# Kernel optimization log

Measured on AMD Instinct MI355X. Metric: run time of the kernel, lower is better.

Reference implementation:

```python
import jax, jax.numpy as jnp
import numpy as np

B, N, C, L = 2, 128, 256, 3
NODE_IN, EDGE_IN = 128, 64
KN, KE = 101, 7
ALPHA = 0.2
EPS = 1e-5

def lrelu(x):
    return jax.nn.leaky_relu(x, ALPHA)

def layer_norm(x, g, b):
    mu = jnp.mean(x, axis=-1, keepdims=True)
    var = jnp.mean((x - mu) ** 2, axis=-1, keepdims=True)
    return (x - mu) / jnp.sqrt(var + EPS) * g + b

def setup_inputs() -> dict:
    key = jax.random.key(0)
    ks = jax.random.split(key, 20)
    s = 0.05
    nodes = jax.random.normal(ks[0], (B, N, NODE_IN), jnp.float32)
    edges = jax.random.normal(ks[1], (B, N, N, EDGE_IN), jnp.float32)
    m = (jax.random.uniform(ks[2], (B, N, N)) > 0.3).astype(jnp.float32)
    adj_mask = jnp.maximum(m, jnp.eye(N, dtype=jnp.float32)[None])  # guarantee non-empty rows
    return {
        'nodes': nodes, 'edges': edges, 'adj_mask': adj_mask,
        'pnW': jax.random.normal(ks[3], (C, NODE_IN)) * s, 'pnb': jnp.zeros((C,)),
        'peW': jax.random.normal(ks[4], (C, EDGE_IN)) * s, 'peb': jnp.zeros((C,)),
        'Wb': jax.random.normal(ks[5], (L, C, 3 * C)) * s,
        'Wbp': jax.random.normal(ks[6], (L, C, C)) * s,
        'Wfp': jax.random.normal(ks[7], (L, C, C)) * s,
        'ub': jax.random.normal(ks[8], (L, C)) * s,
        'Wf': jax.random.normal(ks[9], (L, C, C)) * s,
        'eln_g': jnp.ones((L, C)), 'eln_b': jnp.zeros((L, C)),
        'nln_g': jnp.ones((L, C)), 'nln_b': jnp.zeros((L, C)),
        'ncW': jax.random.normal(ks[10], (KN, C)) * s, 'ncb': jnp.zeros((KN,)),
        'ecW': jax.random.normal(ks[11], (KE, C)) * s, 'ecb': jnp.zeros((KE,)),
    }

def reference(nodes, edges, adj_mask, pnW, pnb, peW, peb, Wb, Wbp, Wfp, ub, Wf,
              eln_g, eln_b, nln_g, nln_b, ncW, ncb, ecW, ecb):
    nodes = nodes @ pnW.T + pnb          # (B,N,C)
    edges = edges @ peW.T + peb          # (B,N,N,C)
    mask3 = adj_mask[..., None]
    for l in range(Wb.shape[0]):
        Cd = nodes.shape[-1]
        Wb1, Wb2, Wb3 = Wb[l][:, :Cd], Wb[l][:, Cd:2 * Cd], Wb[l][:, 2 * Cd:]
        # W_b([f_i, edges, f_j]) without materializing the (B,N,N,3C) concat
        ai = nodes @ Wb1.T                # (B,N,C) broadcast along j
        aj = nodes @ Wb3.T                # (B,N,C) broadcast along i
        ne = lrelu(ai[:, :, None, :] + edges @ Wb2.T + aj[:, None, :, :])
        ne = ne * mask3
        new_edges = layer_norm(ne + edges, eln_g[l], eln_b[l])
        edges_in = jnp.swapaxes(new_edges, 1, 2)      # permute(0,2,1,3)
        tn = nodes @ Wfp[l].T             # shared by term_node_i / term_node_j
        st = edges_in @ Wbp[l].T + tn[:, :, None, :] + tn[:, None, :, :]
        r = lrelu(st @ ub[l])             # (B,N,N)
        r = jnp.where(adj_mask > 0, r, -jnp.inf)
        attn = jnp.nan_to_num(jax.nn.softmax(r, axis=2))
        agg = jnp.einsum('bij,bjd->bid', attn, nodes @ Wf[l].T)
        nodes = layer_norm(lrelu(agg) + nodes, nln_g[l], nln_b[l])
        edges = new_edges
    node_logits = nodes @ ncW.T + ncb
    edge_logits = edges @ ecW.T + ecb
    return (nodes, edges, node_logits, edge_logits)
```

## Files before the change

kernel.cpp:

```cpp
#include <hip/hip_runtime.h>
#include <hip/hip_bf16.h>


#define ALPHA 0.2f
#define EPS_ 1e-5f

typedef __hip_bfloat16 bf16;
typedef __bf16 bf16x8 __attribute__((ext_vector_type(8)));
typedef __bf16 bf16x4 __attribute__((ext_vector_type(4)));
typedef float floatx4 __attribute__((ext_vector_type(4)));

__device__ __forceinline__ float bf2f(bf16 x){ return __bfloat162float(x); }
__device__ __forceinline__ bf16  f2bf(float x){ return __float2bfloat16(x); }
__device__ __forceinline__ float lrelu_f(float x){ return x > 0.f ? x : ALPHA * x; }

#define T_NODES 0u
#define T_EDGES 32768u
#define T_ADJ   2129920u
#define T_PNW   2162688u
#define T_PNB   2195456u
#define T_PEW   2195712u
#define T_PEB   2212096u
#define T_WB    2212352u
#define T_WBP   2802176u
#define T_WFP   2998784u
#define T_UB    3195392u
#define T_WF    3196160u
#define T_ELNG  3392768u
#define T_ELNB  3393536u
#define T_NLNG  3394304u
#define T_NLNB  3395072u
#define T_NCW   3395840u
#define T_NCB   3421696u
#define T_ECW   3421800u
#define T_ECB   3423592u

#define O_NODES 0u
#define O_EDGES 65536u
#define O_NLOG  8454144u
#define O_ELOG  8480000u

struct SrcPtrs { const void* p[20]; };

__device__ __forceinline__ float rawld(const void* p, size_t i, bool isb){
    return isb ? bf2f(((const bf16*)p)[i]) : ((const float*)p)[i];
}

__device__ __forceinline__ bf16x8 ldfrag8(const void* p, size_t e, bool isb){
    if (isb) return *reinterpret_cast<const bf16x8*>((const bf16*)p + e);
    const float4* f = (const float4*)((const float*)p + e);
    float4 a = f[0], b = f[1];
    bf16 o[8];
    o[0]=f2bf(a.x); o[1]=f2bf(a.y); o[2]=f2bf(a.z); o[3]=f2bf(a.w);
    o[4]=f2bf(b.x); o[5]=f2bf(b.y); o[6]=f2bf(b.z); o[7]=f2bf(b.w);
    return *reinterpret_cast<bf16x8*>(o);
}

__global__ __launch_bounds__(256) void setup_k(SrcPtrs sp, bf16* __restrict__ canon,
                                               float* __restrict__ vbuf, float* __restrict__ wbuf,
                                               float* __restrict__ nodes_cur,
                                               bf16* __restrict__ rw2, bf16* __restrict__ rpe){
    const unsigned short* probe = (const unsigned short*)sp.p[12];
    const bool isb = (probe[0] == 0x3F80);
    int blk = blockIdx.x, tid = threadIdx.x;
    int wave = tid >> 6, lane = tid & 63, quad = lane >> 4, l16 = lane & 15;

    if (blk < 1024){
        const unsigned COFF[20] = {T_NODES,T_EDGES,T_ADJ,T_PNW,T_PNB,T_PEW,T_PEB,T_WB,T_WBP,T_WFP,
                                   T_UB,T_WF,T_ELNG,T_ELNB,T_NLNG,T_NLNB,T_NCW,T_NCB,T_ECW,T_ECB};
        const unsigned SZ[20]   = {32768u,2097152u,32768u,32768u,256u,16384u,256u,589824u,196608u,196608u,
                                   768u,196608u,768u,768u,768u,768u,25856u,101u,1792u,7u};
        unsigned gtid = blk*256u + tid;
        unsigned gstride = 1024u*256u;
        for (int t = 0; t < 20; ++t){
            const void* src = sp.p[t];
            unsigned coff = COFF[t], n = SZ[t];
            unsigned chunks = n >> 3;
            if (isb){
                const uint4* s4 = (const uint4*)src;
                for (unsigned idx = gtid; idx < chunks; idx += gstride)
                    *reinterpret_cast<uint4*>(canon + coff + idx*8u) = s4[idx];
            } else {
                const float4* s4 = (const float4*)src;
                for (unsigned idx = gtid; idx < chunks; idx += gstride){
                    float4 a = s4[2*idx], b = s4[2*idx+1];
                    bf16 o[8];
                    o[0]=f2bf(a.x); o[1]=f2bf(a.y); o[2]=f2bf(a.z); o[3]=f2bf(a.w);
                    o[4]=f2bf(b.x); o[5]=f2bf(b.y); o[6]=f2bf(b.z); o[7]=f2bf(b.w);
                    *reinterpret_cast<uint4*>(canon + coff + idx*8u) = *reinterpret_cast<uint4*>(o);
                }
            }
            unsigned tail = n & 7u;
            if (gtid < tail){
                unsigned li = chunks*8u + gtid;
                canon[coff + li] = isb ? ((const bf16*)src)[li] : f2bf(((const float*)src)[li]);
            }
        }
    } else if (blk < 1030){
        int q = blk - 1024;
        int l = q >> 1, m = q & 1;
        const void* W = m ? sp.p[9] : sp.p[8];
        float* out = (m ? wbuf : vbuf) + l*256;
        int c = tid;
        __shared__ float shu[256];
        shu[c] = rawld(sp.p[10], l*256 + c, isb);
        __syncthreads();
        float a0=0.f, a1=0.f, a2=0.f, a3=0.f;
        for (int cp0 = 0; cp0 < 256; cp0 += 16){
#pragma unroll
            for (int j = 0; j < 16; ++j){
                float wv = rawld(W, (size_t)l*65536u + (size_t)(cp0+j)*256u + c, isb);
                float pr = shu[cp0+j] * wv;
                if ((j & 3) == 0) a0 += pr;
                else if ((j & 3) == 1) a1 += pr;
                else if ((j & 3) == 2) a2 += pr;
                else a3 += pr;
            }
        }
        out[c] = (a0 + a1) + (a2 + a3);
    } else if (blk < 1038){
        int row0 = (blk - 1030) * 32;
        floatx4 acc[2][4] = {};
#pragma unroll
        for (int k0c = 0; k0c < 4; ++k0c){
            int k0 = k0c*32;
            bf16x8 a[2], bb[4];
#pragma unroll
            for (int mt = 0; mt < 2; ++mt)
                a[mt] = ldfrag8(sp.p[0], (size_t)(row0 + mt*16 + l16)*128u + k0 + quad*8, isb);
#pragma unroll
            for (int nt = 0; nt < 4; ++nt)
                bb[nt] = ldfrag8(sp.p[3], (size_t)(wave*64 + nt*16 + l16)*128u + k0 + quad*8, isb);
#pragma unroll
            for (int mt = 0; mt < 2; ++mt)
#pragma unroll
                for (int nt = 0; nt < 4; ++nt)
                    acc[mt][nt] = __builtin_amdgcn_mfma_f32_16x16x32_bf16(a[mt], bb[nt], acc[mt][nt], 0, 0, 0);
        }
#pragma unroll
        for (int nt = 0; nt < 4; ++nt){
            int n = wave*64 + nt*16 + l16;
            float bn = rawld(sp.p[4], n, isb);
#pragma unroll
            for (int mt = 0; mt < 2; ++mt)
#pragma unroll
                for (int reg = 0; reg < 4; ++reg){
                    int r = row0 + mt*16 + quad*4 + reg;
                    nodes_cur[r*256 + n] = acc[mt][nt][reg] + bn;
                }
        }
    } else if (blk < 1086){
        int rb = blk - 1038;
        int l = rb >> 4, n_tile = rb & 15;
        bf16* dst = rw2 + l*65536;
#pragma unroll
        for (int half = 0; half < 2; ++half){
            int slot = half*256 + tid;
            int k0c = slot >> 6, ln = slot & 63;
            int qd = ln >> 4, lw = ln & 15;
            int n = n_tile*16 + lw;
            bf16 o[8];
#pragma unroll
            for (int j = 0; j < 8; ++j){
                int k = k0c*32 + qd*8 + j;
                o[j] = f2bf(rawld(sp.p[7], (size_t)l*196608u + (size_t)n*768u + 256u + k, isb));
            }
            *reinterpret_cast<uint4*>(dst + ((n_tile*8 + k0c)*64 + ln)*8) = *reinterpret_cast<uint4*>(o);
        }
    } else {
        int n_tile = blk - 1086;
        if (tid < 128){
            int slot = tid;
            int k0c = slot >> 6, ln = slot & 63;
            int qd = ln >> 4, lw = ln & 15;
            int n = n_tile*16 + lw;
            bf16 o[8];
#pragma unroll
            for (int j = 0; j < 8; ++j){
                int k = k0c*32 + qd*8 + j;
                o[j] = f2bf(rawld(sp.p[5], (size_t)n*64u + k, isb));
            }
            *reinterpret_cast<uint4*>(rpe + ((n_tile*2 + k0c)*64 + ln)*8) = *reinterpret_cast<uint4*>(o);
        }
    }
}

__global__ __launch_bounds__(256) void node_linears_k(
        const float* __restrict__ nodes_cur, const bf16* __restrict__ Wb_l,
        const bf16* __restrict__ Wf_l, const float* __restrict__ w_l,
        float* __restrict__ ai, float* __restrict__ aj,
        float* __restrict__ nf, float* __restrict__ s){
    int row = blockIdx.x;
    int c = threadIdx.x;
    __shared__ float x[256];
    __shared__ float red[4];
    x[c] = nodes_cur[row*256 + c];
    __syncthreads();
    float xs = x[c] * w_l[c];
    for (int off = 32; off; off >>= 1) xs += __shfl_xor(xs, off, 64);
    if ((c & 63) == 0) red[c >> 6] = xs;
    const bf16x8* w1 = reinterpret_cast<const bf16x8*>(Wb_l + (size_t)c*768);
    const bf16x8* w3 = reinterpret_cast<const bf16x8*>(Wb_l + (size_t)c*768 + 512);
    const bf16x8* wf = reinterpret_cast<const bf16x8*>(Wf_l + (size_t)c*256);
    float a1 = 0.f, a3 = 0.f, f = 0.f;
#pragma unroll 4
    for (int ch = 0; ch < 32; ++ch){
        bf16x8 v1 = w1[ch], v3 = w3[ch], vf = wf[ch];
#pragma unroll
        for (int j = 0; j < 8; ++j){
            float xv = x[ch*8 + j];
            a1 += xv * (float)v1[j];
            a3 += xv * (float)v3[j];
            f  += xv * (float)vf[j];
        }
    }
    ai[row*256 + c] = a1;
    aj[row*256 + c] = a3;
    nf[row*256 + c] = f;
    __syncthreads();
    if (c == 0) s[row] = red[0] + red[1] + red[2] + red[3];
}

__global__ __launch_bounds__(256) void edge_update2_k(
        bf16* __restrict__ Ebuf, const bf16* __restrict__ rw2_l,
        const float* __restrict__ ai, const float* __restrict__ aj,
        const bf16* __restrict__ adj, const bf16* __restrict__ g, const bf16* __restrict__ bta,
        const float* __restrict__ v, float* __restrict__ rbuf,
        int isfinal, const bf16* __restrict__ ecW, const bf16* __restrict__ ecb,
        void* __restrict__ dout, const unsigned short* __restrict__ probe,
        int isfirst, const bf16* __restrict__ eIn, const bf16* __restrict__ rpe,
        const bf16* __restrict__ peb){
    int row0 = blockIdx.x * 64;
    int b = row0 >> 14, i = (row0 >> 7) & 127, j0 = row0 & 127;
    int tid = threadIdx.x;
    int wave = tid >> 6, lane = tid & 63, quad = lane >> 4, l16 = lane & 15;

    __shared__ bf16  shA[64*264];
    __shared__ float sh_ai[256];
    __shared__ float sh_v[256];
    __shared__ float sh_g[256];
    __shared__ float sh_bt[256];
    __shared__ float sh_w7[7][256];

    sh_ai[tid] = ai[(b*128 + i)*256 + tid];
    sh_v[tid]  = v[tid];
    sh_g[tid]  = bf2f(g[tid]);
    sh_bt[tid] = bf2f(bta[tid]);
    if (isfirst){
        floatx4 pacc[4][4] = {};
#pragma unroll
        for (int k0c = 0; k0c < 2; ++k0c){
            int k0 = k0c*32;
            bf16x8 a[4], bb[4];
#pragma unroll
            for (int mt = 0; mt < 4; ++mt)
                a[mt] = *reinterpret_cast<const bf16x8*>(eIn + (size_t)(row0 + mt*16 + l16)*64 + k0 + quad*8);
#pragma unroll
            for (int nt = 0; nt < 4; ++nt)
                bb[nt] = *reinterpret_cast<const bf16x8*>(rpe + wave*4096 + nt*1024 + k0c*512 + lane*8);
#pragma unroll
            for (int mt = 0; mt < 4; ++mt)
#pragma unroll
                for (int nt = 0; nt < 4; ++nt)
                    pacc[mt][nt] = __builtin_amdgcn_mfma_f32_16x16x32_bf16(a[mt], bb[nt], pacc[mt][nt], 0, 0, 0);
        }
#pragma unroll
        for (int nt = 0; nt < 4; ++nt){
            int col = wave*64 + nt*16 + l16;
            float bbv = bf2f(peb[col]);
#pragma unroll
            for (int mt = 0; mt < 4; ++mt)
#pragma unroll
                for (int reg = 0; reg < 4; ++reg)
                    shA[(mt*16 + quad*4 + reg)*264 + col] = f2bf(pacc[mt][nt][reg] + bbv);
        }
    } else {
#pragma unroll
        for (int it = 0; it < 8; ++it){
            int idx = it*256 + tid;
            int r = idx >> 5, c8 = idx & 31;
            bf16x8 vA = *reinterpret_cast<const bf16x8*>(Ebuf + (size_t)(row0 + r)*256 + c8*8);
            *reinterpret_cast<bf16x8*>(&shA[r*264 + c8*8]) = vA;
        }
    }
    if (isfinal){
        for (int idx = tid; idx < 7*256; idx += 256)
            sh_w7[idx >> 8][idx & 255] = bf2f(ecW[idx]);
    }
    __syncthreads();

    floatx4 acc[16] = {};
    const bf16* shrow = &shA[(wave*16 + l16)*264];
    for (int k0c = 0; k0c < 8; ++k0c){
        bf16x8 bfrag = *reinterpret_cast<const bf16x8*>(shrow + k0c*32 + quad*8);
#pragma unroll
        for (int mt = 0; mt < 16; ++mt){
            bf16x8 afrag = *reinterpret_cast<const bf16x8*>(rw2_l + (size_t)(mt*8 + k0c)*512 + lane*8);
            acc[mt] = __builtin_amdgcn_mfma_f32_16x16x32_bf16(afrag, bfrag, acc[mt], 0, 0, 0);
        }
    }

    const bool isb = (probe[0] == 0x3F80);
    int rl = wave*16 + l16;
    int j  = j0 + rl;
    int grow = row0 + rl;
    float mask = bf2f(adj[(b*128 + i)*128 + j]);
    const float* ajrow = aj + (size_t)(b*128 + j)*256;

    float sum = 0.f, sumsq = 0.f;
#pragma unroll
    for (int mt = 0; mt < 16; ++mt){
        int c0 = mt*16 + quad*4;
        float4 ajv = *reinterpret_cast<const float4*>(ajrow + c0);
        float4 aiv = *reinterpret_cast<const float4*>(sh_ai + c0);
        bf16x4 ev  = *reinterpret_cast<const bf16x4*>(shrow + c0);
#pragma unroll
        for (int reg = 0; reg < 4; ++reg){
            float y = acc[mt][reg] + ((const float*)&aiv)[reg] + ((const float*)&ajv)[reg];
            float x = lrelu_f(y) * mask + (float)ev[reg];
            acc[mt][reg] = x;
            sum += x; sumsq += x*x;
        }
    }
    sum   += __shfl_xor(sum, 16, 64);   sum   += __shfl_xor(sum, 32, 64);
    sumsq += __shfl_xor(sumsq, 16, 64); sumsq += __shfl_xor(sumsq, 32, 64);
    float mu  = sum * (1.f/256.f);
    float var = sumsq * (1.f/256.f) - mu*mu;
    float rstd = rsqrtf(var + EPS_);

    float dv = 0.f;
    float lg[7] = {0.f,0.f,0.f,0.f,0.f,0.f,0.f};
#pragma unroll
    for (int mt = 0; mt < 16; ++mt){
        int c0 = mt*16 + quad*4;
        float4 gv = *reinterpret_cast<const float4*>(sh_g + c0);
        float4 bv = *reinterpret_cast<const float4*>(sh_bt + c0);
        float4 vv = *reinterpret_cast<const float4*>(sh_v + c0);
        float xo4[4];
#pragma unroll
        for (int reg = 0; reg < 4; ++reg){
            float xo = (acc[mt][reg] - mu) * rstd * ((const float*)&gv)[reg] + ((const float*)&bv)[reg];
            xo4[reg] = xo;
            dv += xo * ((const float*)&vv)[reg];
        }
        if (!isfinal){
            bf16x4 ob;
#pragma unroll
            for (int reg = 0; reg < 4; ++reg) ob[reg] = f2bf(xo4[reg]);
            *reinterpret_cast<bf16x4*>(Ebuf + (size_t)grow*256 + c0) = ob;
        } else {
            if (isb){
                bf16x4 ob;
#pragma unroll
                for (int reg = 0; reg < 4; ++reg) ob[reg] = f2bf(xo4[reg]);
                *reinterpret_cast<bf16x4*>((bf16*)dout + O_EDGES + (size_t)grow*256 + c0) = ob;
            } else {
                float4 of;
                of.x = xo4[0]; of.y = xo4[1]; of.z = xo4[2]; of.w = xo4[3];
                *reinterpret_cast<float4*>((float*)dout + O_EDGES + (size_t)grow*256 + c0) = of;
            }
#pragma unroll
            for (int k = 0; k < 7; ++k){
                const float* w7r = &sh_w7[k][c0];
#pragma unroll
                for (int reg = 0; reg < 4; ++reg) lg[k] += xo4[reg] * w7r[reg];
            }
        }
    }
    dv += __shfl_xor(dv, 16, 64); dv += __shfl_xor(dv, 32, 64);
    if (quad == 0) rbuf[(b*128 + j)*128 + i] = dv;
    if (isfinal){
#pragma unroll
        for (int k = 0; k < 7; ++k){
            lg[k] += __shfl_xor(lg[k], 16, 64);
            lg[k] += __shfl_xor(lg[k], 32, 64);
        }
        if (quad == 0){
#pragma unroll
            for (int k = 0; k < 7; ++k){
                float val = lg[k] + bf2f(ecb[k]);
                if (isb) ((bf16*)dout)[O_ELOG + (size_t)grow*7 + k] = f2bf(val);
                else     ((float*)dout)[O_ELOG + (size_t)grow*7 + k] = val;
            }
        }
    }
}

__global__ __launch_bounds__(256) void node_update_k(
        const float* __restrict__ rbuf, const float* __restrict__ s_in, const bf16* __restrict__ adj,
        const float* __restrict__ nf_in, float* __restrict__ nodes_cur,
        const bf16* __restrict__ g, const bf16* __restrict__ bta,
        int isfinal,
        const bf16* __restrict__ Wb_nx, const bf16* __restrict__ Wf_nx, const float* __restrict__ w_nx,
        float* __restrict__ ai_o, float* __restrict__ aj_o, float* __restrict__ nf_o, float* __restrict__ s_o,
        const bf16* __restrict__ ncW, const bf16* __restrict__ ncb,
        void* __restrict__ dout, const unsigned short* __restrict__ probe){
    int row = blockIdx.x;
    int b = row >> 7;
    int tid = threadIdx.x;
    int wave = tid >> 6, lane = tid & 63;
    __shared__ float attn[128];
    __shared__ float shr[16];
    __shared__ float shfx[256];

    float rv = -__builtin_inff();
    if (tid < 128){
        float t = rbuf[row*128 + tid] + s_in[row] + s_in[b*128 + tid];
        t = lrelu_f(t);
        rv = (bf2f(adj[row*128 + tid]) > 0.f) ? t : -__builtin_inff();
    }
    float m = rv;
    for (int off = 32; off; off >>= 1) m = fmaxf(m, __shfl_xor(m, off, 64));
    if (lane == 0) shr[wave] = m;
    __syncthreads();
    float mx = fmaxf(fmaxf(shr[0], shr[1]), fmaxf(shr[2], shr[3]));
    float e = (tid < 128 && rv > -__builtin_inff()) ? expf(rv - mx) : 0.f;
    if (tid < 128) attn[tid] = e;
    float se = e;
    for (int off = 32; off; off >>= 1) se += __shfl_xor(se, off, 64);
    if (lane == 0) shr[4 + wave] = se;
    __syncthreads();
    float inv = 1.f / (shr[4] + shr[5] + shr[6] + shr[7]);

    int c = tid;
    const float* nfb = nf_in + (size_t)b*128*256 + c;
    float g0 = 0.f, g1 = 0.f, g2 = 0.f, g3 = 0.f;
#pragma unroll 4
    for (int jj = 0; jj < 128; jj += 4){
        g0 += attn[jj]   * nfb[(size_t)jj*256];
        g1 += attn[jj+1] * nfb[(size_t)(jj+1)*256];
        g2 += attn[jj+2] * nfb[(size_t)(jj+2)*256];
        g3 += attn[jj+3] * nfb[(size_t)(jj+3)*256];
    }
    float agg = ((g0 + g1) + (g2 + g3)) * inv;
    float x = lrelu_f(agg) + nodes_cur[row*256 + c];
    float xs = x, xq = x*x;
    for (int off = 32; off; off >>= 1){ xs += __shfl_xor(xs, off, 64); xq += __shfl_xor(xq, off, 64); }
    if (lane == 0){ shr[8 + wave] = xs; shr[12 + wave] = xq; }
    __syncthreads();
    float sum = shr[8] + shr[9] + shr[10] + shr[11];
    float sq  = shr[12] + shr[13] + shr[14] + shr[15];
    float mu  = sum * (1.f/256.f);
    float var = sq * (1.f/256.f) - mu*mu;
    float rstd = rsqrtf(var + EPS_);
    float out = (x - mu) * rstd * bf2f(g[c]) + bf2f(bta[c]);
    nodes_cur[row*256 + c] = out;
    shfx[c] = out;
    __syncthreads();

    if (!isfinal){
        float ws2 = out * w_nx[c];
        for (int off = 32; off; off >>= 1) ws2 += __shfl_xor(ws2, off, 64);
        if (lane == 0) shr[wave] = ws2;
        const bf16x8* w1 = reinterpret_cast<const bf16x8*>(Wb_nx + (size_t)c*768);
        const bf16x8* w3 = reinterpret_cast<const bf16x8*>(Wb_nx + (size_t)c*768 + 512);
        const bf16x8* wf = reinterpret_cast<const bf16x8*>(Wf_nx + (size_t)c*256);
        float a1 = 0.f, a3 = 0.f, f = 0.f;
#pragma unroll 4
        for (int ch = 0; ch < 32; ++ch){
            bf16x8 v1 = w1[ch], v3 = w3[ch], vf = wf[ch];
#pragma unroll
            for (int j = 0; j < 8; ++j){
                float xv = shfx[ch*8 + j];
                a1 += xv * (float)v1[j];
                a3 += xv * (float)v3[j];
                f  += xv * (float)vf[j];
            }
        }
        ai_o[row*256 + c] = a1;
        aj_o[row*256 + c] = a3;
        nf_o[row*256 + c] = f;
        __syncthreads();
        if (c == 0) s_o[row] = shr[0] + shr[1] + shr[2] + shr[3];
    } else {
        const bool isb = (probe[0] == 0x3F80);
        if (isb) ((bf16*)dout)[O_NODES + row*256 + c] = f2bf(out);
        else     ((float*)dout)[O_NODES + row*256 + c] = out;
        if (tid < 101){
            const bf16x8* wr = reinterpret_cast<const bf16x8*>(ncW + (size_t)tid*256);
            float acc = bf2f(ncb[tid]);
#pragma unroll 4
            for (int ch = 0; ch < 32; ++ch){
                bf16x8 wv = wr[ch];
#pragma unroll
                for (int j = 0; j < 8; ++j) acc += shfx[ch*8 + j] * (float)wv[j];
            }
            if (isb) ((bf16*)dout)[O_NLOG + row*101 + tid] = f2bf(acc);
            else     ((float*)dout)[O_NLOG + row*101 + tid] = acc;
        }
    }
}

extern "C" void kernel_launch(void* const* d_in, const int* in_sizes, int n_in,
                              void* d_out, int out_size, void* d_ws, size_t ws_size,
                              hipStream_t stream){
    (void)in_sizes; (void)n_in; (void)out_size; (void)ws_size;

    SrcPtrs sp;
    for (int i = 0; i < 20; ++i) sp.p[i] = d_in[i];
    const unsigned short* probe = (const unsigned short*)d_in[12];

    bf16* canon = (bf16*)d_ws;
    char* ws2 = (char*)d_ws + 6847488;
    bf16* Ebuf = (bf16*)ws2;
    float* f = (float*)(ws2 + 16777216);
    float* ai    = f;
    float* aj    = f + 65536;
    float* nfA   = f + 131072;
    float* nfB   = f + 196608;
    float* sA    = f + 262144;
    float* sB    = f + 262400;
    float* rbuf  = f + 262656;
    float* vbuf  = f + 295424;
    float* wbuf  = f + 296192;
    float* nodes_cur = f + 296960;
    bf16* rw2 = (bf16*)(f + 362496);
    bf16* rpe = rw2 + 196608;

    const bf16* c_edges = canon + T_EDGES;
    const bf16* c_adj   = canon + T_ADJ;
    const bf16* c_peb   = canon + T_PEB;
    const bf16* c_Wb    = canon + T_WB;
    const bf16* c_Wf    = canon + T_WF;
    const bf16* c_elng  = canon + T_ELNG;
    const bf16* c_elnb  = canon + T_ELNB;
    const bf16* c_nlng  = canon + T_NLNG;
    const bf16* c_nlnb  = canon + T_NLNB;
    const bf16* c_ncW   = canon + T_NCW;
    const bf16* c_ncb   = canon + T_NCB;
    const bf16* c_ecW   = canon + T_ECW;
    const bf16* c_ecb   = canon + T_ECB;

    setup_k<<<dim3(1102), dim3(256), 0, stream>>>(sp, canon, vbuf, wbuf, nodes_cur, rw2, rpe);
    node_linears_k<<<dim3(256), dim3(256), 0, stream>>>(
        nodes_cur, c_Wb, c_Wf, wbuf, ai, aj, nfA, sA);

    for (int l = 0; l < 3; ++l){
        int fin = (l == 2);
        int fst = (l == 0);
        float* nf_in = (l & 1) ? nfB : nfA;
        float* nf_out = (l & 1) ? nfA : nfB;
        float* s_in  = (l & 1) ? sB : sA;
        float* s_out = (l & 1) ? sA : sB;
        edge_update2_k<<<dim3(512), dim3(256), 0, stream>>>(
            Ebuf, rw2 + l*65536, ai, aj, c_adj,
            c_elng + l*256, c_elnb + l*256, vbuf + l*256, rbuf,
            fin, c_ecW, c_ecb, d_out, probe,
            fst, c_edges, rpe, c_peb);
        node_update_k <<<dim3(256), dim3(256), 0, stream>>>(
            rbuf, s_in, c_adj, nf_in, nodes_cur, c_nlng + l*256, c_nlnb + l*256,
            fin,
            c_Wb + (size_t)(l+1)*196608, c_Wf + (size_t)(l+1)*65536, wbuf + (l+1)*256,
            ai, aj, nf_out, s_out,
            c_ncW, c_ncb, d_out, probe);
    }
}
```

Baseline: 272.2 us.

## Halve edge-update block to two waves, each reusing weight fragments across two row tiles

```diff
diff --git a/kernel.cpp b/kernel.cpp
--- a/kernel.cpp
+++ b/kernel.cpp
@@ -165,7 +165,7 @@
                 int k = k0c*32 + qd*8 + j;
                 o[j] = f2bf(rawld(sp.p[7], (size_t)l*196608u + (size_t)n*768u + 256u + k, isb));
             }
-            *reinterpret_cast<uint4*>(dst + ((n_tile*8 + k0c)*64 + ln)*8) = *reinterpret_cast<uint4*>(o);
+            *reinterpret_cast<uint4*>(dst + ((k0c*16 + n_tile)*64 + ln)*8) = *reinterpret_cast<uint4*>(o);
         }
     } else {
         int n_tile = blk - 1086;
@@ -221,7 +221,7 @@
     if (c == 0) s[row] = red[0] + red[1] + red[2] + red[3];
 }
 
-__global__ __launch_bounds__(256) void edge_update2_k(
+__global__ __launch_bounds__(128, 2) void edge_update2_k(
         bf16* __restrict__ Ebuf, const bf16* __restrict__ rw2_l,
         const float* __restrict__ ai, const float* __restrict__ aj,
         const bf16* __restrict__ adj, const bf16* __restrict__ g, const bf16* __restrict__ bta,
@@ -242,31 +242,33 @@
     __shared__ float sh_bt[256];
     __shared__ float sh_w7[7][256];
 
-    sh_ai[tid] = ai[(b*128 + i)*256 + tid];
-    sh_v[tid]  = v[tid];
-    sh_g[tid]  = bf2f(g[tid]);
-    sh_bt[tid] = bf2f(bta[tid]);
+    for (int t = tid; t < 256; t += 128){
+        sh_ai[t] = ai[(b*128 + i)*256 + t];
+        sh_v[t]  = v[t];
+        sh_g[t]  = bf2f(g[t]);
+        sh_bt[t] = bf2f(bta[t]);
+    }
     if (isfirst){
-        floatx4 pacc[4][4] = {};
+        floatx4 pacc[4][8] = {};
 #pragma unroll
         for (int k0c = 0; k0c < 2; ++k0c){
             int k0 = k0c*32;
-            bf16x8 a[4], bb[4];
+            bf16x8 a[4], bb[8];
 #pragma unroll
             for (int mt = 0; mt < 4; ++mt)
                 a[mt] = *reinterpret_cast<const bf16x8*>(eIn + (size_t)(row0 + mt*16 + l16)*64 + k0 + quad*8);
 #pragma unroll
-            for (int nt = 0; nt < 4; ++nt)
-                bb[nt] = *reinterpret_cast<const bf16x8*>(rpe + wave*4096 + nt*1024 + k0c*512 + lane*8);
+            for (int nt = 0; nt < 8; ++nt)
+                bb[nt] = *reinterpret_cast<const bf16x8*>(rpe + ((wave*8 + nt)*2 + k0c)*512 + lane*8);
 #pragma unroll
             for (int mt = 0; mt < 4; ++mt)
 #pragma unroll
-                for (int nt = 0; nt < 4; ++nt)
+                for (int nt = 0; nt < 8; ++nt)
                     pacc[mt][nt] = __builtin_amdgcn_mfma_f32_16x16x32_bf16(a[mt], bb[nt], pacc[mt][nt], 0, 0, 0);
         }
 #pragma unroll
-        for (int nt = 0; nt < 4; ++nt){
-            int col = wave*64 + nt*16 + l16;
+        for (int nt = 0; nt < 8; ++nt){
+            int col = wave*128 + nt*16 + l16;
             float bbv = bf2f(peb[col]);
 #pragma unroll
             for (int mt = 0; mt < 4; ++mt)
@@ -276,111 +278,119 @@
         }
     } else {
 #pragma unroll
-        for (int it = 0; it < 8; ++it){
-            int idx = it*256 + tid;
+        for (int it = 0; it < 16; ++it){
+            int idx = it*128 + tid;
             int r = idx >> 5, c8 = idx & 31;
             bf16x8 vA = *reinterpret_cast<const bf16x8*>(Ebuf + (size_t)(row0 + r)*256 + c8*8);
             *reinterpret_cast<bf16x8*>(&shA[r*264 + c8*8]) = vA;
         }
     }
     if (isfinal){
-        for (int idx = tid; idx < 7*256; idx += 256)
+        for (int idx = tid; idx < 7*256; idx += 128)
             sh_w7[idx >> 8][idx & 255] = bf2f(ecW[idx]);
     }
     __syncthreads();
 
-    floatx4 acc[16] = {};
-    const bf16* shrow = &shA[(wave*16 + l16)*264];
+    floatx4 acc[32] = {};
+    const bf16* shrow0 = &shA[(wave*32 + l16)*264];
+    const bf16* shrow1 = shrow0 + 16*264;
     for (int k0c = 0; k0c < 8; ++k0c){
-        bf16x8 bfrag = *reinterpret_cast<const bf16x8*>(shrow + k0c*32 + quad*8);
+        bf16x8 bf0 = *reinterpret_cast<const bf16x8*>(shrow0 + k0c*32 + quad*8);
+        bf16x8 bf1 = *reinterpret_cast<const bf16x8*>(shrow1 + k0c*32 + quad*8);
 #pragma unroll
         for (int mt = 0; mt < 16; ++mt){
-            bf16x8 afrag = *reinterpret_cast<const bf16x8*>(rw2_l + (size_t)(mt*8 + k0c)*512 + lane*8);
-            acc[mt] = __builtin_amdgcn_mfma_f32_16x16x32_bf16(afrag, bfrag, acc[mt], 0, 0, 0);
+            bf16x8 afrag = *reinterpret_cast<const bf16x8*>(rw2_l + (size_t)(k0c*16 + mt)*512 + lane*8);
+            acc[mt]      = __builtin_amdgcn_mfma_f32_16x16x32_bf16(afrag, bf0, acc[mt], 0, 0, 0);
+            acc[16 + mt] = __builtin_amdgcn_mfma_f32_16x16x32_bf16(afrag, bf1, acc[16 + mt], 0, 0, 0);
         }
     }
 
     const bool isb = (probe[0] == 0x3F80);
-    int rl = wave*16 + l16;
-    int j  = j0 + rl;
-    int grow = row0 + rl;
-    float mask = bf2f(adj[(b*128 + i)*128 + j]);
-    const float* ajrow = aj + (size_t)(b*128 + j)*256;
-
-    float sum = 0.f, sumsq = 0.f;
-#pragma unroll
-    for (int mt = 0; mt < 16; ++mt){
-        int c0 = mt*16 + quad*4;
-        float4 ajv = *reinterpret_cast<const float4*>(ajrow + c0);
-        float4 aiv = *reinterpret_cast<const float4*>(sh_ai + c0);
-        bf16x4 ev  = *reinterpret_cast<const bf16x4*>(shrow + c0);
-#pragma unroll
-        for (int reg = 0; reg < 4; ++reg){
-            float y = acc[mt][reg] + ((const float*)&aiv)[reg] + ((const float*)&ajv)[reg];
-            float x = lrelu_f(y) * mask + (float)ev[reg];
-            acc[mt][reg] = x;
-            sum += x; sumsq += x*x;
-        }
-    }
-    sum   += __shfl_xor(sum, 16, 64);   sum   += __shfl_xor(sum, 32, 64);
-    sumsq += __shfl_xor(sumsq, 16, 64); sumsq += __shfl_xor(sumsq, 32, 64);
-    float mu  = sum * (1.f/256.f);
-    float var = sumsq * (1.f/256.f) - mu*mu;
-    float rstd = rsqrtf(var + EPS_);
-
-    float dv = 0.f;
-    float lg[7] = {0.f,0.f,0.f,0.f,0.f,0.f,0.f};
-#pragma unroll
-    for (int mt = 0; mt < 16; ++mt){
-        int c0 = mt*16 + quad*4;
-        float4 gv = *reinterpret_cast<const float4*>(sh_g + c0);
-        float4 bv = *reinterpret_cast<const float4*>(sh_bt + c0);
-        float4 vv = *reinterpret_cast<const float4*>(sh_v + c0);
-        float xo4[4];
-#pragma unroll
-        for (int reg = 0; reg < 4; ++reg){
-            float xo = (acc[mt][reg] - mu) * rstd * ((const float*)&gv)[reg] + ((const float*)&bv)[reg];
-            xo4[reg] = xo;
-            dv += xo * ((const float*)&vv)[reg];
-        }
-        if (!isfinal){
-            bf16x4 ob;
-#pragma unroll
-            for (int reg = 0; reg < 4; ++reg) ob[reg] = f2bf(xo4[reg]);
-            *reinterpret_cast<bf16x4*>(Ebuf + (size_t)grow*256 + c0) = ob;
-        } else {
-            if (isb){
+#pragma unroll
+    for (int r = 0; r < 2; ++r){
+        floatx4* accr = acc + r*16;
+        const bf16* shrow = r ? shrow1 : shrow0;
+        int rl = wave*32 + r*16 + l16;
+        int j  = j0 + rl;
+        int grow = row0 + rl;
+        float mask = bf2f(adj[(b*128 + i)*128 + j]);
+        const float* ajrow = aj + (size_t)(b*128 + j)*256;
+
+        float sum = 0.f, sumsq = 0.f;
+#pragma unroll
+        for (int mt = 0; mt < 16; ++mt){
+            int c0 = mt*16 + quad*4;
+            float4 ajv = *reinterpret_cast<const float4*>(ajrow + c0);
+            float4 aiv = *reinterpret_cast<const float4*>(sh_ai + c0);
+            bf16x4 ev  = *reinterpret_cast<const bf16x4*>(shrow + c0);
+#pragma unroll
+            for (int reg = 0; reg < 4; ++reg){
+                float y = accr[mt][reg] + ((const float*)&aiv)[reg] + ((const float*)&ajv)[reg];
+                float x = lrelu_f(y) * mask + (float)ev[reg];
+                accr[mt][reg] = x;
+                sum += x; sumsq += x*x;
+            }
+        }
+        sum   += __shfl_xor(sum, 16, 64);   sum   += __shfl_xor(sum, 32, 64);
+        sumsq += __shfl_xor(sumsq, 16, 64); sumsq += __shfl_xor(sumsq, 32, 64);
+        float mu  = sum * (1.f/256.f);
+        float var = sumsq * (1.f/256.f) - mu*mu;
+        float rstd = rsqrtf(var + EPS_);
+
+        float dv = 0.f;
+        float lg[7] = {0.f,0.f,0.f,0.f,0.f,0.f,0.f};
+#pragma unroll
+        for (int mt = 0; mt < 16; ++mt){
+            int c0 = mt*16 + quad*4;
+            float4 gv = *reinterpret_cast<const float4*>(sh_g + c0);
+            float4 bv = *reinterpret_cast<const float4*>(sh_bt + c0);
+            float4 vv = *reinterpret_cast<const float4*>(sh_v + c0);
+            float xo4[4];
+#pragma unroll
+            for (int reg = 0; reg < 4; ++reg){
+                float xo = (accr[mt][reg] - mu) * rstd * ((const float*)&gv)[reg] + ((const float*)&bv)[reg];
+                xo4[reg] = xo;
+                dv += xo * ((const float*)&vv)[reg];
+            }
+            if (!isfinal){
                 bf16x4 ob;
 #pragma unroll
                 for (int reg = 0; reg < 4; ++reg) ob[reg] = f2bf(xo4[reg]);
-                *reinterpret_cast<bf16x4*>((bf16*)dout + O_EDGES + (size_t)grow*256 + c0) = ob;
+                *reinterpret_cast<bf16x4*>(Ebuf + (size_t)grow*256 + c0) = ob;
             } else {
-                float4 of;
-                of.x = xo4[0]; of.y = xo4[1]; of.z = xo4[2]; of.w = xo4[3];
-                *reinterpret_cast<float4*>((float*)dout + O_EDGES + (size_t)grow*256 + c0) = of;
-            }
+                if (isb){
+                    bf16x4 ob;
+#pragma unroll
+                    for (int reg = 0; reg < 4; ++reg) ob[reg] = f2bf(xo4[reg]);
+                    *reinterpret_cast<bf16x4*>((bf16*)dout + O_EDGES + (size_t)grow*256 + c0) = ob;
+                } else {
+                    float4 of;
+                    of.x = xo4[0]; of.y = xo4[1]; of.z = xo4[2]; of.w = xo4[3];
+                    *reinterpret_cast<float4*>((float*)dout + O_EDGES + (size_t)grow*256 + c0) = of;
+                }
+#pragma unroll
+                for (int k = 0; k < 7; ++k){
+                    const float* w7r = &sh_w7[k][c0];
+#pragma unroll
+                    for (int reg = 0; reg < 4; ++reg) lg[k] += xo4[reg] * w7r[reg];
+                }
+            }
+        }
+        dv += __shfl_xor(dv, 16, 64); dv += __shfl_xor(dv, 32, 64);
+        if (quad == 0) rbuf[(b*128 + j)*128 + i] = dv;
+        if (isfinal){
 #pragma unroll
             for (int k = 0; k < 7; ++k){
-                const float* w7r = &sh_w7[k][c0];
-#pragma unroll
-                for (int reg = 0; reg < 4; ++reg) lg[k] += xo4[reg] * w7r[reg];
-            }
-        }
-    }
-    dv += __shfl_xor(dv, 16, 64); dv += __shfl_xor(dv, 32, 64);
-    if (quad == 0) rbuf[(b*128 + j)*128 + i] = dv;
-    if (isfinal){
-#pragma unroll
-        for (int k = 0; k < 7; ++k){
-            lg[k] += __shfl_xor(lg[k], 16, 64);
-            lg[k] += __shfl_xor(lg[k], 32, 64);
-        }
-        if (quad == 0){
-#pragma unroll
-            for (int k = 0; k < 7; ++k){
-                float val = lg[k] + bf2f(ecb[k]);
-                if (isb) ((bf16*)dout)[O_ELOG + (size_t)grow*7 + k] = f2bf(val);
-                else     ((float*)dout)[O_ELOG + (size_t)grow*7 + k] = val;
+                lg[k] += __shfl_xor(lg[k], 16, 64);
+                lg[k] += __shfl_xor(lg[k], 32, 64);
+            }
+            if (quad == 0){
+#pragma unroll
+                for (int k = 0; k < 7; ++k){
+                    float val = lg[k] + bf2f(ecb[k]);
+                    if (isb) ((bf16*)dout)[O_ELOG + (size_t)grow*7 + k] = f2bf(val);
+                    else     ((float*)dout)[O_ELOG + (size_t)grow*7 + k] = val;
+                }
             }
         }
     }
@@ -423,16 +433,20 @@
     float inv = 1.f / (shr[4] + shr[5] + shr[6] + shr[7]);
 
     int c = tid;
-    const float* nfb = nf_in + (size_t)b*128*256 + c;
+    const float* nfb = nf_in + (size_t)b*32768 + c;
     float g0 = 0.f, g1 = 0.f, g2 = 0.f, g3 = 0.f;
-#pragma unroll 4
-    for (int jj = 0; jj < 128; jj += 4){
+    float g4 = 0.f, g5 = 0.f, g6 = 0.f, g7 = 0.f;
+    for (int jj = 0; jj < 128; jj += 8){
         g0 += attn[jj]   * nfb[(size_t)jj*256];
         g1 += attn[jj+1] * nfb[(size_t)(jj+1)*256];
         g2 += attn[jj+2] * nfb[(size_t)(jj+2)*256];
         g3 += attn[jj+3] * nfb[(size_t)(jj+3)*256];
-    }
-    float agg = ((g0 + g1) + (g2 + g3)) * inv;
+        g4 += attn[jj+4] * nfb[(size_t)(jj+4)*256];
+        g5 += attn[jj+5] * nfb[(size_t)(jj+5)*256];
+        g6 += attn[jj+6] * nfb[(size_t)(jj+6)*256];
+        g7 += attn[jj+7] * nfb[(size_t)(jj+7)*256];
+    }
+    float agg = (((g0 + g1) + (g2 + g3)) + ((g4 + g5) + (g6 + g7))) * inv;
     float x = lrelu_f(agg) + nodes_cur[row*256 + c];
     float xs = x, xq = x*x;
     for (int off = 32; off; off >>= 1){ xs += __shfl_xor(xs, off, 64); xq += __shfl_xor(xq, off, 64); }
@@ -542,7 +556,7 @@
         float* nf_out = (l & 1) ? nfA : nfB;
         float* s_in  = (l & 1) ? sB : sA;
         float* s_out = (l & 1) ? sA : sB;
-        edge_update2_k<<<dim3(512), dim3(256), 0, stream>>>(
+        edge_update2_k<<<dim3(512), dim3(128), 0, stream>>>(
             Ebuf, rw2 + l*65536, ai, aj, c_adj,
             c_elng + l*256, c_elnb + l*256, vbuf + l*256, rbuf,
             fin, c_ecW, c_ecb, d_out, probe,
```

Measured after the change: 344.1 us. +26.4%, slower.

## Split edge GEMM output channels across waves to reuse weight fragments

Applied to the files above, without the earlier changes.

```diff
diff --git a/kernel.cpp b/kernel.cpp
--- a/kernel.cpp
+++ b/kernel.cpp
@@ -165,7 +165,7 @@
                 int k = k0c*32 + qd*8 + j;
                 o[j] = f2bf(rawld(sp.p[7], (size_t)l*196608u + (size_t)n*768u + 256u + k, isb));
             }
-            *reinterpret_cast<uint4*>(dst + ((n_tile*8 + k0c)*64 + ln)*8) = *reinterpret_cast<uint4*>(o);
+            *reinterpret_cast<uint4*>(dst + ((k0c*16 + n_tile)*64 + ln)*8) = *reinterpret_cast<uint4*>(o);
         }
     } else {
         int n_tile = blk - 1086;
@@ -241,6 +241,10 @@
     __shared__ float sh_g[256];
     __shared__ float sh_bt[256];
     __shared__ float sh_w7[7][256];
+    __shared__ float smS[4][64];
+    __shared__ float smQ[4][64];
+    __shared__ float dvp[4][64];
+    __shared__ float lgp[4][64][7];
 
     sh_ai[tid] = ai[(b*128 + i)*256 + tid];
     sh_v[tid]  = v[tid];
@@ -257,7 +261,7 @@
                 a[mt] = *reinterpret_cast<const bf16x8*>(eIn + (size_t)(row0 + mt*16 + l16)*64 + k0 + quad*8);
 #pragma unroll
             for (int nt = 0; nt < 4; ++nt)
-                bb[nt] = *reinterpret_cast<const bf16x8*>(rpe + wave*4096 + nt*1024 + k0c*512 + lane*8);
+                bb[nt] = *reinterpret_cast<const bf16x8*>(rpe + ((size_t)((wave*4 + nt)*2 + k0c)*64 + lane)*8);
 #pragma unroll
             for (int mt = 0; mt < 4; ++mt)
 #pragma unroll
@@ -289,98 +293,134 @@
     }
     __syncthreads();
 
-    floatx4 acc[16] = {};
-    const bf16* shrow = &shA[(wave*16 + l16)*264];
-    for (int k0c = 0; k0c < 8; ++k0c){
-        bf16x8 bfrag = *reinterpret_cast<const bf16x8*>(shrow + k0c*32 + quad*8);
-#pragma unroll
-        for (int mt = 0; mt < 16; ++mt){
-            bf16x8 afrag = *reinterpret_cast<const bf16x8*>(rw2_l + (size_t)(mt*8 + k0c)*512 + lane*8);
-            acc[mt] = __builtin_amdgcn_mfma_f32_16x16x32_bf16(afrag, bfrag, acc[mt], 0, 0, 0);
+    floatx4 acc[4][4] = {};
+    {
+        const bf16* shb = &shA[l16*264];
+        for (int k0c = 0; k0c < 8; ++k0c){
+            bf16x8 bfr[4];
+#pragma unroll
+            for (int rf = 0; rf < 4; ++rf)
+                bfr[rf] = *reinterpret_cast<const bf16x8*>(shb + rf*16*264 + k0c*32 + quad*8);
+#pragma unroll
+            for (int mt = 0; mt < 4; ++mt){
+                bf16x8 afrag = *reinterpret_cast<const bf16x8*>(
+                    rw2_l + ((size_t)(k0c*16 + wave*4 + mt)*64 + lane)*8);
+#pragma unroll
+                for (int rf = 0; rf < 4; ++rf)
+                    acc[mt][rf] = __builtin_amdgcn_mfma_f32_16x16x32_bf16(afrag, bfr[rf], acc[mt][rf], 0, 0, 0);
+            }
         }
     }
 
     const bool isb = (probe[0] == 0x3F80);
-    int rl = wave*16 + l16;
-    int j  = j0 + rl;
-    int grow = row0 + rl;
-    float mask = bf2f(adj[(b*128 + i)*128 + j]);
-    const float* ajrow = aj + (size_t)(b*128 + j)*256;
-
-    float sum = 0.f, sumsq = 0.f;
-#pragma unroll
-    for (int mt = 0; mt < 16; ++mt){
-        int c0 = mt*16 + quad*4;
-        float4 ajv = *reinterpret_cast<const float4*>(ajrow + c0);
-        float4 aiv = *reinterpret_cast<const float4*>(sh_ai + c0);
-        bf16x4 ev  = *reinterpret_cast<const bf16x4*>(shrow + c0);
-#pragma unroll
-        for (int reg = 0; reg < 4; ++reg){
-            float y = acc[mt][reg] + ((const float*)&aiv)[reg] + ((const float*)&ajv)[reg];
-            float x = lrelu_f(y) * mask + (float)ev[reg];
-            acc[mt][reg] = x;
-            sum += x; sumsq += x*x;
-        }
-    }
-    sum   += __shfl_xor(sum, 16, 64);   sum   += __shfl_xor(sum, 32, 64);
-    sumsq += __shfl_xor(sumsq, 16, 64); sumsq += __shfl_xor(sumsq, 32, 64);
-    float mu  = sum * (1.f/256.f);
-    float var = sumsq * (1.f/256.f) - mu*mu;
-    float rstd = rsqrtf(var + EPS_);
-
-    float dv = 0.f;
-    float lg[7] = {0.f,0.f,0.f,0.f,0.f,0.f,0.f};
-#pragma unroll
-    for (int mt = 0; mt < 16; ++mt){
-        int c0 = mt*16 + quad*4;
-        float4 gv = *reinterpret_cast<const float4*>(sh_g + c0);
-        float4 bv = *reinterpret_cast<const float4*>(sh_bt + c0);
-        float4 vv = *reinterpret_cast<const float4*>(sh_v + c0);
-        float xo4[4];
-#pragma unroll
-        for (int reg = 0; reg < 4; ++reg){
-            float xo = (acc[mt][reg] - mu) * rstd * ((const float*)&gv)[reg] + ((const float*)&bv)[reg];
-            xo4[reg] = xo;
-            dv += xo * ((const float*)&vv)[reg];
-        }
-        if (!isfinal){
-            bf16x4 ob;
-#pragma unroll
-            for (int reg = 0; reg < 4; ++reg) ob[reg] = f2bf(xo4[reg]);
-            *reinterpret_cast<bf16x4*>(Ebuf + (size_t)grow*256 + c0) = ob;
-        } else {
-            if (isb){
+    float maskv[4];
+#pragma unroll
+    for (int rf = 0; rf < 4; ++rf){
+        int rl = rf*16 + l16;
+        int j  = j0 + rl;
+        maskv[rf] = bf2f(adj[(b*128 + i)*128 + j]);
+        const float* ajrow = aj + (size_t)(b*128 + j)*256;
+        float s = 0.f, q = 0.f;
+#pragma unroll
+        for (int mt = 0; mt < 4; ++mt){
+            int c0 = wave*64 + mt*16 + quad*4;
+            float4 ajv = *reinterpret_cast<const float4*>(ajrow + c0);
+            float4 aiv = *reinterpret_cast<const float4*>(sh_ai + c0);
+            bf16x4 ev  = *reinterpret_cast<const bf16x4*>(&shA[rl*264 + c0]);
+#pragma unroll
+            for (int reg = 0; reg < 4; ++reg){
+                float y = acc[mt][rf][reg] + ((const float*)&aiv)[reg] + ((const float*)&ajv)[reg];
+                float x = lrelu_f(y) * maskv[rf] + (float)ev[reg];
+                acc[mt][rf][reg] = x;
+                s += x; q += x*x;
+            }
+        }
+        s += __shfl_xor(s, 16, 64); s += __shfl_xor(s, 32, 64);
+        q += __shfl_xor(q, 16, 64); q += __shfl_xor(q, 32, 64);
+        if (quad == 0){ smS[wave][rl] = s; smQ[wave][rl] = q; }
+    }
+    __syncthreads();
+
+#pragma unroll
+    for (int rf = 0; rf < 4; ++rf){
+        int rl = rf*16 + l16;
+        int j  = j0 + rl;
+        int grow = row0 + rl;
+        float ts = smS[0][rl] + smS[1][rl] + smS[2][rl] + smS[3][rl];
+        float tq = smQ[0][rl] + smQ[1][rl] + smQ[2][rl] + smQ[3][rl];
+        float mu  = ts * (1.f/256.f);
+        float var = tq * (1.f/256.f) - mu*mu;
+        float rstd = rsqrtf(var + EPS_);
+        float dv = 0.f;
+        float lg[7] = {0.f,0.f,0.f,0.f,0.f,0.f,0.f};
+#pragma unroll
+        for (int mt = 0; mt < 4; ++mt){
+            int c0 = wave*64 + mt*16 + quad*4;
+            float4 gv = *reinterpret_cast<const float4*>(sh_g + c0);
+            float4 bv = *reinterpret_cast<const float4*>(sh_bt + c0);
+            float4 vv = *reinterpret_cast<const float4*>(sh_v + c0);
+            float xo4[4];
+#pragma unroll
+            for (int reg = 0; reg < 4; ++reg){
+                float xo = (acc[mt][rf][reg] - mu) * rstd * ((const float*)&gv)[reg] + ((const float*)&bv)[reg];
+                xo4[reg] = xo;
+                dv += xo * ((const float*)&vv)[reg];
+            }
+            if (!isfinal){
                 bf16x4 ob;
 #pragma unroll
                 for (int reg = 0; reg < 4; ++reg) ob[reg] = f2bf(xo4[reg]);
-                *reinterpret_cast<bf16x4*>((bf16*)dout + O_EDGES + (size_t)grow*256 + c0) = ob;
+                *reinterpret_cast<bf16x4*>(Ebuf + (size_t)grow*256 + c0) = ob;
             } else {
-                float4 of;
-                of.x = xo4[0]; of.y = xo4[1]; of.z = xo4[2]; of.w = xo4[3];
-                *reinterpret_cast<float4*>((float*)dout + O_EDGES + (size_t)grow*256 + c0) = of;
-            }
+                if (isb){
+                    bf16x4 ob;
+#pragma unroll
+                    for (int reg = 0; reg < 4; ++reg) ob[reg] = f2bf(xo4[reg]);
+                    *reinterpret_cast<bf16x4*>((bf16*)dout + O_EDGES + (size_t)grow*256 + c0) = ob;
+                } else {
+                    float4 of;
+                    of.x = xo4[0]; of.y = xo4[1]; of.z = xo4[2]; of.w = xo4[3];
+                    *reinterpret_cast<float4*>((float*)dout + O_EDGES + (size_t)grow*256 + c0) = of;
+                }
+#pragma unroll
+                for (int k = 0; k < 7; ++k){
+                    const float* w7r = &sh_w7[k][c0];
+#pragma unroll
+                    for (int reg = 0; reg < 4; ++reg) lg[k] += xo4[reg] * w7r[reg];
+                }
+            }
+        }
+        dv += __shfl_xor(dv, 16, 64); dv += __shfl_xor(dv, 32, 64);
+        if (quad == 0) dvp[wave][rl] = dv;
+        if (isfinal){
 #pragma unroll
             for (int k = 0; k < 7; ++k){
-                const float* w7r = &sh_w7[k][c0];
-#pragma unroll
-                for (int reg = 0; reg < 4; ++reg) lg[k] += xo4[reg] * w7r[reg];
-            }
-        }
-    }
-    dv += __shfl_xor(dv, 16, 64); dv += __shfl_xor(dv, 32, 64);
-    if (quad == 0) rbuf[(b*128 + j)*128 + i] = dv;
-    if (isfinal){
-#pragma unroll
-        for (int k = 0; k < 7; ++k){
-            lg[k] += __shfl_xor(lg[k], 16, 64);
-            lg[k] += __shfl_xor(lg[k], 32, 64);
-        }
-        if (quad == 0){
-#pragma unroll
-            for (int k = 0; k < 7; ++k){
-                float val = lg[k] + bf2f(ecb[k]);
-                if (isb) ((bf16*)dout)[O_ELOG + (size_t)grow*7 + k] = f2bf(val);
-                else     ((float*)dout)[O_ELOG + (size_t)grow*7 + k] = val;
+                lg[k] += __shfl_xor(lg[k], 16, 64);
+                lg[k] += __shfl_xor(lg[k], 32, 64);
+            }
+            if (quad == 0){
+#pragma unroll
+                for (int k = 0; k < 7; ++k) lgp[wave][rl][k] = lg[k];
+            }
+        }
+    }
+    __syncthreads();
+
+    if (wave == 0 && quad == 0){
+#pragma unroll
+        for (int rf = 0; rf < 4; ++rf){
+            int rl = rf*16 + l16;
+            int j  = j0 + rl;
+            int grow = row0 + rl;
+            float d = dvp[0][rl] + dvp[1][rl] + dvp[2][rl] + dvp[3][rl];
+            rbuf[(b*128 + j)*128 + i] = d;
+            if (isfinal){
+#pragma unroll
+                for (int k = 0; k < 7; ++k){
+                    float val = lgp[0][rl][k] + lgp[1][rl][k] + lgp[2][rl][k] + lgp[3][rl][k] + bf2f(ecb[k]);
+                    if (isb) ((bf16*)dout)[O_ELOG + (size_t)grow*7 + k] = f2bf(val);
+                    else     ((float*)dout)[O_ELOG + (size_t)grow*7 + k] = val;
+                }
             }
         }
     }
@@ -423,16 +463,20 @@
     float inv = 1.f / (shr[4] + shr[5] + shr[6] + shr[7]);
 
     int c = tid;
-    const float* nfb = nf_in + (size_t)b*128*256 + c;
+    const float* nfb = nf_in + (size_t)b*32768 + c;
     float g0 = 0.f, g1 = 0.f, g2 = 0.f, g3 = 0.f;
-#pragma unroll 4
-    for (int jj = 0; jj < 128; jj += 4){
+    float g4 = 0.f, g5 = 0.f, g6 = 0.f, g7 = 0.f;
+    for (int jj = 0; jj < 128; jj += 8){
         g0 += attn[jj]   * nfb[(size_t)jj*256];
         g1 += attn[jj+1] * nfb[(size_t)(jj+1)*256];
         g2 += attn[jj+2] * nfb[(size_t)(jj+2)*256];
         g3 += attn[jj+3] * nfb[(size_t)(jj+3)*256];
-    }
-    float agg = ((g0 + g1) + (g2 + g3)) * inv;
+        g4 += attn[jj+4] * nfb[(size_t)(jj+4)*256];
+        g5 += attn[jj+5] * nfb[(size_t)(jj+5)*256];
+        g6 += attn[jj+6] * nfb[(size_t)(jj+6)*256];
+        g7 += attn[jj+7] * nfb[(size_t)(jj+7)*256];
+    }
+    float agg = (((g0 + g1) + (g2 + g3)) + ((g4 + g5) + (g6 + g7))) * inv;
     float x = lrelu_f(agg) + nodes_cur[row*256 + c];
     float xs = x, xq = x*x;
     for (int off = 32; off; off >>= 1){ xs += __shfl_xor(xs, off, 64); xq += __shfl_xor(xq, off, 64); }
```

After: 274.5 us. About the same (+0.9%).
